# Kernel optimization log

Measured on AMD Instinct MI355X. Metric: run time of the kernel, lower is better.

## Reference

```python
import jax, jax.numpy as jnp
import numpy as np
import math

IN_C = 512
OUT_C = 512
K = 3
STYLE = 512
EPS = 1e-8
MOD_SCALE = 1.0 / math.sqrt(STYLE)        # EqualLinear scale (lr_mul=1)
CONV_SCALE = 1.0 / math.sqrt(IN_C * K * K)  # ModulatedConv2d scale


def setup_inputs() -> dict:
    key = jax.random.key(0)
    k1, k2, k3, k4 = jax.random.split(key, 4)
    return {
        "x": jax.random.normal(k1, (8, IN_C, 64, 64), dtype=jnp.float32),
        "style": jax.random.normal(k2, (8, STYLE), dtype=jnp.float32),
        "mod_weight": jax.random.normal(k3, (IN_C, STYLE), dtype=jnp.float32),
        "mod_bias": jnp.ones((IN_C,), dtype=jnp.float32),
        "weight": jax.random.normal(k4, (1, OUT_C, IN_C, K, K), dtype=jnp.float32),
    }


def _per_sample_conv(xi, wi):
    # xi: [in_c, H, W], wi: [out_c, in_c, K, K]
    out = jax.lax.conv_general_dilated(
        xi[None], wi, window_strides=(1, 1), padding="SAME",
        dimension_numbers=("NCHW", "OIHW", "NCHW"))
    return out[0]


def reference(x, style, mod_weight, mod_bias, weight):
    # EqualLinear modulation: s = style @ (W*scale)^T + bias  -> [B, in_c]
    s = style @ (mod_weight * MOD_SCALE).T + mod_bias
    # per-sample modulated weight: [B, out_c, in_c, K, K]
    w = CONV_SCALE * weight * s[:, None, :, None, None]
    demod = jax.lax.rsqrt(jnp.sum(w * w, axis=(2, 3, 4), keepdims=True) + EPS)
    w = w * demod
    # grouped conv (groups=batch) == vmap of per-sample conv
    out = jax.vmap(_per_sample_conv)(x, w)  # [B, out_c, H, W]
    return out
```

## Files before the change

### kernel.cpp

```cpp
#include <hip/hip_runtime.h>
#include <hip/hip_bf16.h>

typedef __attribute__((ext_vector_type(8))) short bf16x8;
typedef __attribute__((ext_vector_type(16))) float f32x16;
typedef unsigned int u32;

#define MOD_SCALE 0.04419417382415922f
#define CONV_SCALE 0.014731391274719742f

__device__ __forceinline__ unsigned short f2bf(float f) {
  union { float f; u32 u; } v; v.f = f;
  u32 r = v.u + 0x7fffu + ((v.u >> 16) & 1u);
  return (unsigned short)(r >> 16);
}

__device__ __forceinline__ void gload_lds16(const void* g, void* l) {
  __builtin_amdgcn_global_load_lds(
      (const __attribute__((address_space(1))) u32*)g,
      (__attribute__((address_space(3))) u32*)l, 16, 0, 0);
}

__global__ void k_prep(const float* __restrict__ wsrc, ushort* __restrict__ wb,
                       float* __restrict__ wsq, float* __restrict__ zerobuf,
                       const float* __restrict__ style, const float* __restrict__ mw,
                       const float* __restrict__ mb, float* __restrict__ s) {
  __shared__ float wtile[2304];
  const int t = threadIdx.x;
  if (blockIdx.x < 1024) {
    const float4* s4 = (const float4*)(wsrc + (size_t)blockIdx.x * 2304);
    float4* w4 = (float4*)wtile;
    w4[t] = s4[t];
    w4[t + 256] = s4[t + 256];
    if (t < 64) w4[t + 512] = s4[t + 512];
    __syncthreads();
    int idx = blockIdx.x * 256 + t;
    int oc = idx >> 9, ic = idx & 511;
    int icb = ic >> 4, icr = ic & 15;
    if (blockIdx.x == 0 && t < 16) zerobuf[t] = 0.f;
    float sq = 0.f;
    #pragma unroll
    for (int tap = 0; tap < 9; ++tap) {
      float v = wtile[t * 9 + tap];
      sq += v * v;
      wb[((tap * 32 + icb) * 512 + oc) * 16 + icr] = f2bf(v);
    }
    wsq[idx] = sq;
  } else {
    int idx = (blockIdx.x - 1024) * 256 + t;
    int b = idx >> 9, ic = idx & 511;
    const float4* wr = (const float4*)(mw + ic * 512);
    const float4* sr = (const float4*)(style + b * 512);
    float acc = 0.f;
    #pragma unroll 4
    for (int k = 0; k < 128; ++k) {
      float4 a = wr[k], c = sr[k];
      acc += a.x * c.x + a.y * c.y + a.z * c.z + a.w * c.w;
    }
    s[idx] = acc * MOD_SCALE + mb[ic];
  }
}

__global__ void k_xform(const float* __restrict__ x, const float* __restrict__ s,
                        ushort* __restrict__ xsb, const float* __restrict__ wsq,
                        float* __restrict__ dscale) {
  __shared__ float red[256];
  const int t = threadIdx.x;
  const int y = blockIdx.x & 63, b = blockIdx.x >> 6;
  const int px = t & 63, icq = t >> 6;
  #pragma unroll
  for (int i = 0; i < 8; ++i) {
    int icb = i * 4 + icq;
    union { ushort u[16]; uint4 v[2]; } pk;
    #pragma unroll
    for (int j = 0; j < 16; ++j) {
      int ic = icb * 16 + j;
      float v = x[(b * 512 + ic) * 4096 + y * 64 + px] * s[b * 512 + ic];
      pk.u[j] = f2bf(v);
    }
    ushort* dst = xsb + ((size_t)((b * 64 + y) * 32 + icb) * 64 + px) * 16;
    *(uint4*)dst = pk.v[0];
    *(uint4*)(dst + 8) = pk.v[1];
  }
  if (y < 8) {
    const int oc_l = t & 63, kq = t >> 6;
    const float4* wq = (const float4*)(wsq + (size_t)(y * 64 + oc_l) * 512) + kq * 32;
    const float4* sp = (const float4*)(s + b * 512) + kq * 32;
    float part = 0.f;
    #pragma unroll 4
    for (int k = 0; k < 32; ++k) {
      float4 a = wq[k], c = sp[k];
      part += a.x * c.x * c.x + a.y * c.y * c.y + a.z * c.z * c.z + a.w * c.w * c.w;
    }
    red[t] = part;
    __syncthreads();
    if (t < 64)
      dscale[b * 512 + y * 64 + t] = CONV_SCALE * rsqrtf(
          CONV_SCALE * CONV_SCALE * (red[t] + red[t + 64] + red[t + 128] + red[t + 192]) + 1e-8f);
  }
}

#define ABYTES 18432
#define BUFB   39552
#define SMEMSZ (2 * BUFB + 256)
__global__ __launch_bounds__(256, 2) void k_conv(
    const ushort* __restrict__ wb, const ushort* __restrict__ xsb,
    const float* __restrict__ dscale, const float* __restrict__ zerobuf,
    float* __restrict__ out) {
  const int yb = blockIdx.x, ocb = blockIdx.y, b = blockIdx.z;
  const int t = threadIdx.x;
  const int wv = t >> 6, l = t & 63;
  const int lc = l & 31, lh = l >> 5;
  const int wvr = wv >> 1, wvp = wv & 1;
  const int y0 = yb * 8, oc0 = ocb * 64;

  extern __shared__ char smem[];
  float* dss = (float*)(smem + 2 * BUFB);
  if (t < 64) dss[t] = dscale[b * 512 + oc0 + t];

  f32x16 acc[4][2];
  #pragma unroll
  for (int rr = 0; rr < 4; ++rr)
    #pragma unroll
    for (int ocf = 0; ocf < 2; ++ocf)
      #pragma unroll
      for (int k = 0; k < 16; ++k)
        acc[rr][ocf][k] = 0.f;

  const char* asrc[5];
  #pragma unroll
  for (int i = 0; i < 5; ++i) {
    int cid = i * 256 + t;
    int tap = cid >> 7, cc = cid & 127;
    int oc_l = cc >> 1, h = cc & 1;
    asrc[i] = (const char*)wb + (size_t)tap * 524288 + (size_t)(oc0 + oc_l) * 32 + h * 16;
  }
  const char* bsrc[6];
  int bstride[6];
  #pragma unroll
  for (int i = 0; i < 6; ++i) {
    int cid = i * 256 + t;
    int r = cid / 132, rem = cid - r * 132;
    int yy = y0 - 1 + r;
    bool interior = (rem >= 2) && (rem < 130) && ((unsigned)yy < 64u);
    bsrc[i] = interior
        ? (const char*)xsb + (size_t)(b * 64 + yy) * 65536 + (rem - 2) * 16
        : (const char*)zerobuf;
    bstride[i] = interior ? 2048 : 0;
  }

  const int apo = (lc * 2 + lh) * 16;
  const int bco = (wvp * 32 + lc) * 32 + lh * 16;

  auto STAGE = [&](int bo, int icb) {
    char* Ab = smem + bo;
    char* Bb = Ab + ABYTES;
    const int aoff = icb * 16384;
    #pragma unroll
    for (int i = 0; i < 4; ++i)
      gload_lds16(asrc[i] + aoff, Ab + i * 4096 + wv * 1024);
    if (t < 128)
      gload_lds16(asrc[4] + aoff, Ab + 16384 + wv * 1024);
    #pragma unroll
    for (int i = 0; i < 5; ++i)
      gload_lds16(bsrc[i] + icb * bstride[i], Bb + i * 4096 + wv * 1024);
    if (t < 40)
      gload_lds16(bsrc[5] + icb * bstride[5], Bb + 20480);
  };

  auto COMPUTE = [&](int bo) {
    const char* Ab = smem + bo;
    const char* Bb = smem + bo + ABYTES;
    #pragma unroll
    for (int dx = 0; dx < 3; ++dx) {
      bf16x8 bfr[6];
      #pragma unroll
      for (int j = 0; j < 6; ++j)
        bfr[j] = *(const bf16x8*)(Bb + (wvr * 4 + j) * 2112 + dx * 32 + bco);
      bf16x8 af[3][2];
      #pragma unroll
      for (int dy = 0; dy < 3; ++dy)
        #pragma unroll
        for (int ocf = 0; ocf < 2; ++ocf)
          af[dy][ocf] = *(const bf16x8*)(Ab + (dy * 3 + dx) * 2048 + ocf * 1024 + apo);
      #pragma unroll
      for (int dy = 0; dy < 3; ++dy)
        #pragma unroll
        for (int rr = 0; rr < 4; ++rr)
          #pragma unroll
          for (int ocf = 0; ocf < 2; ++ocf)
            acc[rr][ocf] = __builtin_amdgcn_mfma_f32_32x32x16_bf16(
                af[dy][ocf], bfr[rr + dy], acc[rr][ocf], 0, 0, 0);
    }
  };

  STAGE(0, 0);
  __syncthreads();
  #pragma unroll 1
  for (int it = 0; it < 32; it += 2) {
    STAGE(BUFB, it + 1);
    COMPUTE(0);
    __syncthreads();
    if (it < 30) STAGE(0, it + 2);
    COMPUTE(BUFB);
    __syncthreads();
  }

  #pragma unroll
  for (int rr = 0; rr < 4; ++rr) {
    const int y_row = y0 + wvr * 4 + rr;
    #pragma unroll
    for (int ocf = 0; ocf < 2; ++ocf) {
      #pragma unroll
      for (int reg = 0; reg < 16; ++reg) {
        int oc_l = ocf * 32 + (reg & 3) + 8 * (reg >> 2) + 4 * lh;
        out[(size_t)(b * 512 + oc0 + oc_l) * 4096 + y_row * 64 + wvp * 32 + lc]
            = acc[rr][ocf][reg] * dss[oc_l];
      }
    }
  }
}

extern "C" void kernel_launch(void* const* d_in, const int* in_sizes, int n_in,
                              void* d_out, int out_size, void* d_ws, size_t ws_size,
                              hipStream_t stream) {
  const float* x     = (const float*)d_in[0];
  const float* style = (const float*)d_in[1];
  const float* mw    = (const float*)d_in[2];
  const float* mb    = (const float*)d_in[3];
  const float* wsrc  = (const float*)d_in[4];
  float* out = (float*)d_out;

  char* ws = (char*)d_ws;
  float*  zerobuf = (float*)(ws + 0);
  float*  s       = (float*)(ws + 256);
  float*  dscale  = (float*)(ws + 16640);
  float*  wsq     = (float*)(ws + 33024);
  ushort* wb      = (ushort*)(ws + 1081600);
  ushort* xsb     = (ushort*)(ws + 5800192);

  hipFuncSetAttribute(reinterpret_cast<const void*>(k_conv),
                      hipFuncAttributeMaxDynamicSharedMemorySize, SMEMSZ);

  k_prep<<<dim3(1040), dim3(256), 0, stream>>>(wsrc, wb, wsq, zerobuf, style, mw, mb, s);
  k_xform<<<dim3(512), dim3(256), 0, stream>>>(x, s, xsb, wsq, dscale);
  k_conv<<<dim3(8, 8, 8), dim3(256), SMEMSZ, stream>>>(wb, xsb, dscale, zerobuf, out);
}
```

Baseline: 172.0 us.

## Move demodulation reduction into conv kernel and split xform grid over channels

The per-output-channel demodulation sum, previously computed by a subset of k_xform blocks, is now computed inside k_conv right after the first stage load, so the prologue load latency can hide it. k_xform no longer has the imbalanced y<8 tail and is launched with twice as many blocks, each handling half the input channels, to improve parallelism on the memory-bound transform. The cost is redundant demod work: each of the 8 y-blocks of k_conv recomputes the same 64-channel reduction. There is also slightly more LDS per block.

```diff
diff --git a/kernel.cpp b/kernel.cpp
--- a/kernel.cpp
+++ b/kernel.cpp
@@ -61,15 +61,13 @@
 }
 
 __global__ void k_xform(const float* __restrict__ x, const float* __restrict__ s,
-                        ushort* __restrict__ xsb, const float* __restrict__ wsq,
-                        float* __restrict__ dscale) {
-  __shared__ float red[256];
+                        ushort* __restrict__ xsb) {
+  const int y = blockIdx.x, b = blockIdx.y, ich = blockIdx.z;
   const int t = threadIdx.x;
-  const int y = blockIdx.x & 63, b = blockIdx.x >> 6;
   const int px = t & 63, icq = t >> 6;
   #pragma unroll
-  for (int i = 0; i < 8; ++i) {
-    int icb = i * 4 + icq;
+  for (int i = 0; i < 4; ++i) {
+    int icb = ich * 16 + i * 4 + icq;
     union { ushort u[16]; uint4 v[2]; } pk;
     #pragma unroll
     for (int j = 0; j < 16; ++j) {
@@ -81,31 +79,17 @@
     *(uint4*)dst = pk.v[0];
     *(uint4*)(dst + 8) = pk.v[1];
   }
-  if (y < 8) {
-    const int oc_l = t & 63, kq = t >> 6;
-    const float4* wq = (const float4*)(wsq + (size_t)(y * 64 + oc_l) * 512) + kq * 32;
-    const float4* sp = (const float4*)(s + b * 512) + kq * 32;
-    float part = 0.f;
-    #pragma unroll 4
-    for (int k = 0; k < 32; ++k) {
-      float4 a = wq[k], c = sp[k];
-      part += a.x * c.x * c.x + a.y * c.y * c.y + a.z * c.z * c.z + a.w * c.w * c.w;
-    }
-    red[t] = part;
-    __syncthreads();
-    if (t < 64)
-      dscale[b * 512 + y * 64 + t] = CONV_SCALE * rsqrtf(
-          CONV_SCALE * CONV_SCALE * (red[t] + red[t + 64] + red[t + 128] + red[t + 192]) + 1e-8f);
-  }
 }
 
 #define ABYTES 18432
 #define BUFB   39552
-#define SMEMSZ (2 * BUFB + 256)
+#define REDOFF (2 * BUFB)
+#define DSSOFF (2 * BUFB + 1024)
+#define SMEMSZ (2 * BUFB + 1024 + 256)
 __global__ __launch_bounds__(256, 2) void k_conv(
     const ushort* __restrict__ wb, const ushort* __restrict__ xsb,
-    const float* __restrict__ dscale, const float* __restrict__ zerobuf,
-    float* __restrict__ out) {
+    const float* __restrict__ wsq, const float* __restrict__ s,
+    const float* __restrict__ zerobuf, float* __restrict__ out) {
   const int yb = blockIdx.x, ocb = blockIdx.y, b = blockIdx.z;
   const int t = threadIdx.x;
   const int wv = t >> 6, l = t & 63;
@@ -114,8 +98,8 @@
   const int y0 = yb * 8, oc0 = ocb * 64;
 
   extern __shared__ char smem[];
-  float* dss = (float*)(smem + 2 * BUFB);
-  if (t < 64) dss[t] = dscale[b * 512 + oc0 + t];
+  float* red = (float*)(smem + REDOFF);
+  float* dss = (float*)(smem + DSSOFF);
 
   f32x16 acc[4][2];
   #pragma unroll
@@ -194,7 +178,23 @@
   };
 
   STAGE(0, 0);
+  {
+    const int oc_l = t & 63, kq = t >> 6;
+    const float4* wq = (const float4*)(wsq + (size_t)(oc0 + oc_l) * 512) + kq * 32;
+    const float4* sp = (const float4*)(s + b * 512) + kq * 32;
+    float part = 0.f;
+    #pragma unroll 4
+    for (int k = 0; k < 32; ++k) {
+      float4 a = wq[k], c = sp[k];
+      part += a.x * c.x * c.x + a.y * c.y * c.y + a.z * c.z * c.z + a.w * c.w * c.w;
+    }
+    red[t] = part;
+  }
   __syncthreads();
+  if (t < 64)
+    dss[t] = CONV_SCALE * rsqrtf(
+        CONV_SCALE * CONV_SCALE * (red[t] + red[t + 64] + red[t + 128] + red[t + 192]) + 1e-8f);
+
   #pragma unroll 1
   for (int it = 0; it < 32; it += 2) {
     STAGE(BUFB, it + 1);
@@ -233,7 +233,6 @@
   char* ws = (char*)d_ws;
   float*  zerobuf = (float*)(ws + 0);
   float*  s       = (float*)(ws + 256);
-  float*  dscale  = (float*)(ws + 16640);
   float*  wsq     = (float*)(ws + 33024);
   ushort* wb      = (ushort*)(ws + 1081600);
   ushort* xsb     = (ushort*)(ws + 5800192);
@@ -242,6 +241,6 @@
                       hipFuncAttributeMaxDynamicSharedMemorySize, SMEMSZ);
 
   k_prep<<<dim3(1040), dim3(256), 0, stream>>>(wsrc, wb, wsq, zerobuf, style, mw, mb, s);
-  k_xform<<<dim3(512), dim3(256), 0, stream>>>(x, s, xsb, wsq, dscale);
-  k_conv<<<dim3(8, 8, 8), dim3(256), SMEMSZ, stream>>>(wb, xsb, dscale, zerobuf, out);
-}
+  k_xform<<<dim3(64, 8, 2), dim3(256), 0, stream>>>(x, s, xsb);
+  k_conv<<<dim3(8, 8, 8), dim3(256), SMEMSZ, stream>>>(wb, xsb, wsq, s, zerobuf, out);
+}
```

After: 173.4 us. No clear change (+0.8%).

## Share weight tile across two batch samples per 512-thread conv block

Applied to the files above, without the earlier changes.

Each conv block now processes two batch samples with 8 waves, loading the modulated-weight A tile once into LDS and using it for both samples' activation tiles. This halves global weight traffic per output and the number of blocks, with launch bounds moving from 256x2 to 512x1. The cost is larger LDS use per block (about 121KB double-buffered), fewer blocks (256), and possibly lower occupancy and latency hiding.

```diff
diff --git a/kernel.cpp b/kernel.cpp
--- a/kernel.cpp
+++ b/kernel.cpp
@@ -100,22 +100,24 @@
 }
 
 #define ABYTES 18432
-#define BUFB   39552
-#define SMEMSZ (2 * BUFB + 256)
-__global__ __launch_bounds__(256, 2) void k_conv(
+#define BBYTES 21120
+#define BUFB   (ABYTES + 2 * BBYTES)
+#define SMEMSZ (2 * BUFB + 512)
+__global__ __launch_bounds__(512, 1) void k_conv(
     const ushort* __restrict__ wb, const ushort* __restrict__ xsb,
     const float* __restrict__ dscale, const float* __restrict__ zerobuf,
     float* __restrict__ out) {
-  const int yb = blockIdx.x, ocb = blockIdx.y, b = blockIdx.z;
+  const int yb = blockIdx.x, ocb = blockIdx.y, bp = blockIdx.z;
   const int t = threadIdx.x;
   const int wv = t >> 6, l = t & 63;
   const int lc = l & 31, lh = l >> 5;
-  const int wvr = wv >> 1, wvp = wv & 1;
-  const int y0 = yb * 8, oc0 = ocb * 64;
+  const int bb = wv >> 2, wloc = wv & 3;
+  const int wvr = wloc >> 1, wvp = wloc & 1;
+  const int y0 = yb * 8, oc0 = ocb * 64, b0 = bp * 2;
 
   extern __shared__ char smem[];
   float* dss = (float*)(smem + 2 * BUFB);
-  if (t < 64) dss[t] = dscale[b * 512 + oc0 + t];
+  if (t < 128) dss[t] = dscale[(b0 + (t >> 6)) * 512 + oc0 + (t & 63)];
 
   f32x16 acc[4][2];
   #pragma unroll
@@ -126,24 +128,26 @@
       for (int k = 0; k < 16; ++k)
         acc[rr][ocf][k] = 0.f;
 
-  const char* asrc[5];
-  #pragma unroll
-  for (int i = 0; i < 5; ++i) {
-    int cid = i * 256 + t;
+  const char* asrc[3];
+  #pragma unroll
+  for (int i = 0; i < 3; ++i) {
+    int cid = i * 512 + t;
     int tap = cid >> 7, cc = cid & 127;
-    int oc_l = cc >> 1, h = cc & 1;
-    asrc[i] = (const char*)wb + (size_t)tap * 524288 + (size_t)(oc0 + oc_l) * 32 + h * 16;
+    if (tap > 8) tap = 8;
+    asrc[i] = (const char*)wb + (size_t)tap * 524288 + (size_t)(oc0 + (cc >> 1)) * 32 + (cc & 1) * 16;
   }
   const char* bsrc[6];
   int bstride[6];
   #pragma unroll
   for (int i = 0; i < 6; ++i) {
-    int cid = i * 256 + t;
-    int r = cid / 132, rem = cid - r * 132;
+    int cid = i * 512 + t;
+    int bat = cid >= 1320;
+    int c = cid - bat * 1320;
+    int r = c / 132, rem = c - r * 132;
     int yy = y0 - 1 + r;
-    bool interior = (rem >= 2) && (rem < 130) && ((unsigned)yy < 64u);
+    bool interior = (rem >= 2) && (rem < 130) && ((unsigned)yy < 64u) && (cid < 2640);
     bsrc[i] = interior
-        ? (const char*)xsb + (size_t)(b * 64 + yy) * 65536 + (rem - 2) * 16
+        ? (const char*)xsb + (size_t)((b0 + bat) * 64 + yy) * 65536 + (rem - 2) * 16
         : (const char*)zerobuf;
     bstride[i] = interior ? 2048 : 0;
   }
@@ -156,20 +160,20 @@
     char* Bb = Ab + ABYTES;
     const int aoff = icb * 16384;
     #pragma unroll
-    for (int i = 0; i < 4; ++i)
-      gload_lds16(asrc[i] + aoff, Ab + i * 4096 + wv * 1024);
+    for (int i = 0; i < 2; ++i)
+      gload_lds16(asrc[i] + aoff, Ab + i * 8192 + wv * 1024);
     if (t < 128)
-      gload_lds16(asrc[4] + aoff, Ab + 16384 + wv * 1024);
+      gload_lds16(asrc[2] + aoff, Ab + 16384 + wv * 1024);
     #pragma unroll
     for (int i = 0; i < 5; ++i)
-      gload_lds16(bsrc[i] + icb * bstride[i], Bb + i * 4096 + wv * 1024);
-    if (t < 40)
-      gload_lds16(bsrc[5] + icb * bstride[5], Bb + 20480);
+      gload_lds16(bsrc[i] + icb * bstride[i], Bb + i * 8192 + wv * 1024);
+    if (t < 80)
+      gload_lds16(bsrc[5] + icb * bstride[5], Bb + 40960 + wv * 1024);
   };
 
   auto COMPUTE = [&](int bo) {
     const char* Ab = smem + bo;
-    const char* Bb = smem + bo + ABYTES;
+    const char* Bb = smem + bo + ABYTES + bb * BBYTES;
     #pragma unroll
     for (int dx = 0; dx < 3; ++dx) {
       bf16x8 bfr[6];
@@ -205,6 +209,7 @@
     __syncthreads();
   }
 
+  const int b = b0 + bb;
   #pragma unroll
   for (int rr = 0; rr < 4; ++rr) {
     const int y_row = y0 + wvr * 4 + rr;
@@ -214,7 +219,7 @@
       for (int reg = 0; reg < 16; ++reg) {
         int oc_l = ocf * 32 + (reg & 3) + 8 * (reg >> 2) + 4 * lh;
         out[(size_t)(b * 512 + oc0 + oc_l) * 4096 + y_row * 64 + wvp * 32 + lc]
-            = acc[rr][ocf][reg] * dss[oc_l];
+            = acc[rr][ocf][reg] * dss[bb * 64 + oc_l];
       }
     }
   }
@@ -243,5 +248,5 @@
 
   k_prep<<<dim3(1040), dim3(256), 0, stream>>>(wsrc, wb, wsq, zerobuf, style, mw, mb, s);
   k_xform<<<dim3(512), dim3(256), 0, stream>>>(x, s, xsb, wsq, dscale);
-  k_conv<<<dim3(8, 8, 8), dim3(256), SMEMSZ, stream>>>(wb, xsb, dscale, zerobuf, out);
-}
+  k_conv<<<dim3(8, 8, 4), dim3(512), SMEMSZ, stream>>>(wb, xsb, dscale, zerobuf, out);
+}
```

Result: no change. 172.2 us (+0.1%).
